# Optimization experiments

Measured on AMD Instinct MI355X. Metric: run time of the kernel, lower is better.

Reference implementation:

```python
import jax, jax.numpy as jnp
import numpy as np

H, DH, ITERS, EPS, LN_EPS = 8, 32, 3, 1e-8, 1e-5

def _ln(x, w, b):
    m = jnp.mean(x, axis=-1, keepdims=True)
    v = jnp.mean(jnp.square(x - m), axis=-1, keepdims=True)
    return (x - m) * jax.lax.rsqrt(v + LN_EPS) * w + b

def setup_inputs() -> dict:
    key = jax.random.key(0)
    ks = jax.random.split(key, 16)
    B, N, D, S = 64, 4096, 256, 8
    DI = H * DH  # 256
    HID = max(D, 128)
    s = 0.02
    return {
        "inputs": jax.random.normal(ks[0], (B, N, D), jnp.float32),
        "noise": jax.random.normal(ks[1], (B, S, D), jnp.float32),
        "slots_mean": jax.random.normal(ks[2], (1, 1, D), jnp.float32),
        "slots_logvar": jax.random.normal(ks[3], (1, 1, D), jnp.float32) * s,
        "wq": jax.random.normal(ks[4], (D, DI), jnp.float32) * s,
        "bq": jnp.zeros((DI,), jnp.float32),
        "wk": jax.random.normal(ks[5], (D, DI), jnp.float32) * s,
        "bk": jnp.zeros((DI,), jnp.float32),
        "wv": jax.random.normal(ks[6], (D, DI), jnp.float32) * s,
        "bv": jnp.zeros((DI,), jnp.float32),
        "wo": jax.random.normal(ks[7], (DI, D), jnp.float32) * s,
        "bo": jnp.zeros((D,), jnp.float32),
        "w_ih": jax.random.normal(ks[8], (D, 3 * D), jnp.float32) * s,
        "b_ih": jnp.zeros((3 * D,), jnp.float32),
        "w_hh": jax.random.normal(ks[9], (D, 3 * D), jnp.float32) * s,
        "b_hh": jnp.zeros((3 * D,), jnp.float32),
        "w1": jax.random.normal(ks[10], (D, HID), jnp.float32) * s,
        "b1": jnp.zeros((HID,), jnp.float32),
        "w2": jax.random.normal(ks[11], (HID, D), jnp.float32) * s,
        "b2": jnp.zeros((D,), jnp.float32),
        "ln_in_w": jnp.ones((D,), jnp.float32), "ln_in_b": jnp.zeros((D,), jnp.float32),
        "ln_s_w": jnp.ones((D,), jnp.float32), "ln_s_b": jnp.zeros((D,), jnp.float32),
        "ln_ff_w": jnp.ones((D,), jnp.float32), "ln_ff_b": jnp.zeros((D,), jnp.float32),
    }

def reference(inputs, noise, slots_mean, slots_logvar, wq, bq, wk, bk, wv, bv,
              wo, bo, w_ih, b_ih, w_hh, b_hh, w1, b1, w2, b2,
              ln_in_w, ln_in_b, ln_s_w, ln_s_b, ln_ff_w, ln_ff_b):
    B, N, D = inputs.shape
    S = noise.shape[1]
    scale = D ** -0.5  # note: scale uses dim, per original code
    # slot init: mean + exp(logvar) * noise (faithful: exp(logvar) used directly)
    slots = slots_mean + jnp.exp(slots_logvar) * noise  # [B,S,D]
    x = _ln(inputs, ln_in_w, ln_in_b)
    k = (x @ wk + bk).reshape(B, N, H, DH).transpose(0, 2, 1, 3)  # [B,H,N,Dh]
    v = (x @ wv + bv).reshape(B, N, H, DH).transpose(0, 2, 1, 3)
    attn = None
    for _ in range(ITERS):
        slots_prev = slots
        s = _ln(slots, ln_s_w, ln_s_b)
        q = (s @ wq + bq).reshape(B, S, H, DH).transpose(0, 2, 1, 3)  # [B,H,S,Dh]
        dots = jnp.einsum('bhid,bhjd->bhij', q, k) * scale  # [B,H,S,N]
        attn = jax.nn.softmax(dots, axis=-2)  # softmax over slot axis
        attn = attn + EPS
        attn = attn / jnp.clip(jnp.sum(attn, axis=-1, keepdims=True), 1e-12)  # L1 over inputs
        upd = jnp.einsum('bhjd,bhij->bhid', v, attn)  # [B,H,S,Dh]
        upd = upd.transpose(0, 2, 1, 3).reshape(B, S, H * DH) @ wo + bo  # [B,S,D]
        # GRUCell (torch gate order r,z,n)
        xg = upd.reshape(B * S, D) @ w_ih + b_ih
        hg = slots_prev.reshape(B * S, D) @ w_hh + b_hh
        xr, xz, xn = jnp.split(xg, 3, axis=-1)
        hr, hz, hn = jnp.split(hg, 3, axis=-1)
        r = jax.nn.sigmoid(xr + hr)
        z = jax.nn.sigmoid(xz + hz)
        n = jnp.tanh(xn + r * hn)
        slots = ((1.0 - z) * n + z * slots_prev.reshape(B * S, D)).reshape(B, S, D)
        ff = _ln(slots, ln_ff_w, ln_ff_b)
        slots = slots + (jax.nn.relu(ff @ w1 + b1) @ w2 + b2)
    return slots, attn
```

## Files before the change

kernel.cpp:

```cpp
#include <hip/hip_runtime.h>
#include <stdint.h>

typedef __attribute__((ext_vector_type(8))) short bf16x8;
typedef __attribute__((ext_vector_type(4))) float f32x4;

__device__ __forceinline__ float b2f(unsigned short s) {
    unsigned int u = ((unsigned int)s) << 16;
    return __builtin_bit_cast(float, u);
}
__device__ __forceinline__ unsigned short f2b(float f) {
    unsigned int u = __builtin_bit_cast(unsigned int, f);
    u += 0x7FFFu + ((u >> 16) & 1u);
    return (unsigned short)(u >> 16);
}
__device__ __forceinline__ void unpack8(uint4 u, float* o) {
    unsigned int a0 = u.x, a1 = u.y, a2 = u.z, a3 = u.w;
    o[0] = __builtin_bit_cast(float, a0 << 16);
    o[1] = __builtin_bit_cast(float, a0 & 0xffff0000u);
    o[2] = __builtin_bit_cast(float, a1 << 16);
    o[3] = __builtin_bit_cast(float, a1 & 0xffff0000u);
    o[4] = __builtin_bit_cast(float, a2 << 16);
    o[5] = __builtin_bit_cast(float, a2 & 0xffff0000u);
    o[6] = __builtin_bit_cast(float, a3 << 16);
    o[7] = __builtin_bit_cast(float, a3 & 0xffff0000u);
}

#define GLOAD_LDS16(g, l) __builtin_amdgcn_global_load_lds( \
    (const __attribute__((address_space(1))) unsigned int*)(g), \
    (__attribute__((address_space(3))) unsigned int*)(l), 16, 0, 0)

#define EPS_ATTN 1e-8f
#define LN_EPS 1e-5f
#define SCALE 0.0625f

__global__ __launch_bounds__(256) void k_prep(const float* __restrict__ wk,
                                              const float* __restrict__ wv,
                                              unsigned short* __restrict__ W3) {
    int g = blockIdx.x * 256 + threadIdx.x;
    int j = g & 7;
    int f = (g >> 3) & 1023;
    int stage = g >> 13;
    int p = f & 15, qq = (f >> 4) & 3, ntl = f >> 6;
    int kc = stage >> 1, half = stage & 1;
    int k = kc * 32 + qq * 8 + j;
    int n = half * 256 + ntl * 16 + p;
    float v = (n < 256) ? wk[k * 256 + n] : wv[k * 256 + (n - 256)];
    W3[g] = f2b(v);
}

__global__ __launch_bounds__(256) void k_init(const float* __restrict__ sm,
                                              const float* __restrict__ slv,
                                              const float* __restrict__ noise,
                                              float* __restrict__ slots) {
    int idx = blockIdx.x * 256 + threadIdx.x;
    int d = idx & 255;
    slots[idx] = sm[d] + expf(slv[d]) * noise[idx];
}

__global__ __launch_bounds__(256, 2) void k_kv(
    const float* __restrict__ x, const float* __restrict__ lnw, const float* __restrict__ lnb,
    const unsigned short* __restrict__ W3, const float* __restrict__ bk, const float* __restrict__ bv,
    unsigned short* __restrict__ Kb, unsigned short* __restrict__ Vb) {
    __shared__ __align__(16) unsigned short sh[33792];
    unsigned short* As = sh;
    unsigned short* Bs = sh + 16384;
    float* bL = (float*)(sh + 32768);
    int t = threadIdx.x;
    int w = t >> 6, lane = t & 63;
    int p = lane & 15, q = lane >> 4;

    {
        const unsigned short* gp = W3 + (size_t)(w * 4) * 512 + lane * 8;
        #pragma unroll
        for (int c = 0; c < 4; ++c)
            GLOAD_LDS16(gp + c * 512, Bs + (w * 4 + c) * 512);
    }
    if (t < 128) {
        float4 bb = (t < 64) ? ((const float4*)bk)[t] : ((const float4*)bv)[t - 64];
        *(float4*)&bL[t * 4] = bb;
    }

    float4 lw  = ((const float4*)lnw)[lane];
    float4 lbv = ((const float4*)lnb)[lane];
    float4 xv[16];
    const float* xbase = x + ((size_t)blockIdx.x * 64 + w * 16) * 256;
    #pragma unroll
    for (int i = 0; i < 16; ++i) xv[i] = ((const float4*)(xbase + i * 256))[lane];
    int kcw = lane >> 3, qw = (lane >> 1) & 3, j0 = (lane & 1) * 4;
    #pragma unroll
    for (int i = 0; i < 16; ++i) {
        float4 v = xv[i];
        float s0 = v.x + v.y + v.z + v.w;
        float s1 = v.x * v.x + v.y * v.y + v.z * v.z + v.w * v.w;
        #pragma unroll
        for (int o = 1; o < 64; o <<= 1) { s0 += __shfl_xor(s0, o); s1 += __shfl_xor(s1, o); }
        float mean = s0 * (1.0f / 256.0f);
        float var  = s1 * (1.0f / 256.0f) - mean * mean;
        float rstd = rsqrtf(var + LN_EPS);
        ushort4 pk;
        pk.x = f2b((v.x - mean) * rstd * lw.x + lbv.x);
        pk.y = f2b((v.y - mean) * rstd * lw.y + lbv.y);
        pk.z = f2b((v.z - mean) * rstd * lw.z + lbv.z);
        pk.w = f2b((v.w - mean) * rstd * lw.w + lbv.w);
        int pos = (qw * 16 + i) ^ kcw;
        *(ushort4*)&As[((w * 8 + kcw) * 64 + pos) * 8 + j0] = pk;
    }
    __syncthreads();

    f32x4 acc[32];
    f32x4 zero = {0.f, 0.f, 0.f, 0.f};
    #pragma unroll
    for (int i = 0; i < 32; ++i) acc[i] = zero;

    for (int s1 = 0; s1 < 16; ++s1) {
        if (s1 < 15) {
            int nx = s1 + 1;
            const unsigned short* gp = W3 + (size_t)nx * 8192 + (w * 4) * 512 + lane * 8;
            unsigned short* lb = Bs + ((nx & 1) ? 8192 : 0);
            #pragma unroll
            for (int c = 0; c < 4; ++c)
                GLOAD_LDS16(gp + c * 512, lb + (w * 4 + c) * 512);
        }
        int kc = s1 >> 1, half = s1 & 1;
        bf16x8 af = *(const bf16x8*)&As[((w * 8 + kc) * 64 + ((q * 16 + p) ^ kc)) * 8];
        const unsigned short* bbuf = Bs + ((s1 & 1) ? 8192 : 0);
        #pragma unroll
        for (int ntl = 0; ntl < 16; ++ntl) {
            bf16x8 bf = *(const bf16x8*)&bbuf[ntl * 512 + lane * 8];
            acc[half * 16 + ntl] = __builtin_amdgcn_mfma_f32_16x16x32_bf16(
                af, bf, acc[half * 16 + ntl], 0, 0, 0);
        }
        __syncthreads();
    }

    unsigned short* rep = As;
    int b_   = blockIdx.x >> 6;
    int n0g  = (blockIdx.x & 63) * 64;

    #pragma unroll
    for (int al = 0; al < 16; ++al) {
        float bias = bL[al * 16 + p];
        int hl = al >> 1, dh = (al & 1) * 16 + p;
        #pragma unroll
        for (int r = 0; r < 4; ++r) {
            int nl = w * 16 + q * 4 + r;
            rep[(hl * 64 + nl) * 32 + dh] = f2b(acc[al][r] + bias);
        }
    }
    __syncthreads();
    #pragma unroll
    for (int i = 0; i < 8; ++i) {
        uint4 vd = *(const uint4*)&rep[(i * 256 + t) * 8];
        *(uint4*)(Kb + (((size_t)b_ * 8 + i) * 4096 + n0g) * 32 + t * 8) = vd;
    }
    #pragma unroll
    for (int al = 0; al < 16; ++al) {
        float bias = bL[256 + al * 16 + p];
        int hl = al >> 1, dh = (al & 1) * 16 + p;
        ushort4 pk;
        pk.x = f2b(acc[16 + al][0] + bias);
        pk.y = f2b(acc[16 + al][1] + bias);
        pk.z = f2b(acc[16 + al][2] + bias);
        pk.w = f2b(acc[16 + al][3] + bias);
        *(ushort4*)(Vb + ((size_t)(b_ * 8 + hl) * 32 + dh) * 4096 + n0g + w * 16 + q * 4) = pk;
    }
}

__global__ __launch_bounds__(256) void k_q(
    const float* __restrict__ slots, const float* __restrict__ lnw, const float* __restrict__ lnb,
    const float* __restrict__ wq, const float* __restrict__ bq, float* __restrict__ qg) {
    __shared__ float sln[256];
    __shared__ float red[8];
    int t = threadIdx.x;
    int row = blockIdx.x;
    float v = slots[(size_t)row * 256 + t];
    float s0 = v, s1 = v * v;
    #pragma unroll
    for (int off = 1; off < 64; off <<= 1) { s0 += __shfl_xor(s0, off); s1 += __shfl_xor(s1, off); }
    if ((t & 63) == 0) { red[t >> 6] = s0; red[4 + (t >> 6)] = s1; }
    __syncthreads();
    float ts0 = red[0] + red[1] + red[2] + red[3];
    float ts1 = red[4] + red[5] + red[6] + red[7];
    float mean = ts0 * (1.f / 256.f);
    float var  = ts1 * (1.f / 256.f) - mean * mean;
    float rstd = rsqrtf(var + LN_EPS);
    sln[t] = (v - mean) * rstd * lnw[t] + lnb[t];
    __syncthreads();
    float acc = bq[t];
    #pragma unroll 4
    for (int k = 0; k < 256; ++k) acc += sln[k] * wq[k * 256 + t];
    int b = row >> 3, sl = row & 7;
    qg[(size_t)b * 2048 + (t >> 5) * 256 + sl * 32 + (t & 31)] = acc;
}

__global__ __launch_bounds__(512) void k_attn(
    const unsigned short* __restrict__ Kg, const unsigned short* __restrict__ VTg,
    const float* __restrict__ qg, float* __restrict__ upd_raw, float* __restrict__ rowsum,
    float* __restrict__ attn_out, int last) {
    __shared__ float supd[8][256];
    __shared__ float srs[8][8];
    int t = threadIdx.x;
    int w = t >> 6, lane = t & 63;
    int c = lane & 15;
    int g = lane >> 4;

    int bh = blockIdx.x;
    const unsigned short* Kbh = Kg  + (size_t)bh * 4096 * 32;
    const unsigned short* Vbh = VTg + (size_t)bh * 32 * 4096;

    bf16x8 qhi = {0,0,0,0,0,0,0,0};
    bf16x8 qlo = {0,0,0,0,0,0,0,0};
    if (c < 8) {
        const float* qp = qg + (size_t)bh * 256 + c * 32 + g * 8;
        #pragma unroll
        for (int j = 0; j < 8; ++j) {
            float qv = qp[j];
            unsigned short hb = f2b(qv);
            qhi[j] = (short)hb;
            qlo[j] = (short)f2b(qv - b2f(hb));
        }
    }

    f32x4 zero = {0.f, 0.f, 0.f, 0.f};
    f32x4 accL = zero, accH = zero;
    float rs = 0.f;
    int nb0 = w * 512;

    #pragma unroll 2
    for (int pr = 0; pr < 16; ++pr) {
        int base = nb0 + pr * 32;
        bf16x8 k0 = *(const bf16x8*)(Kbh + (size_t)(base + c) * 32 + g * 8);
        bf16x8 k1 = *(const bf16x8*)(Kbh + (size_t)(base + 16 + c) * 32 + g * 8);
        const unsigned short* vlo = Vbh + (size_t)c * 4096 + base + g * 4;
        const unsigned short* vhi = Vbh + (size_t)(c + 16) * 4096 + base + g * 4;
        union { ushort4 h[2]; bf16x8 v; } V0, V1;
        V0.h[0] = *(const ushort4*)vlo;
        V0.h[1] = *(const ushort4*)(vlo + 16);
        V1.h[0] = *(const ushort4*)vhi;
        V1.h[1] = *(const ushort4*)(vhi + 16);

        f32x4 s0 = __builtin_amdgcn_mfma_f32_16x16x32_bf16(k0, qhi, zero, 0, 0, 0);
        s0 = __builtin_amdgcn_mfma_f32_16x16x32_bf16(k0, qlo, s0, 0, 0, 0);
        f32x4 s1 = __builtin_amdgcn_mfma_f32_16x16x32_bf16(k1, qhi, zero, 0, 0, 0);
        s1 = __builtin_amdgcn_mfma_f32_16x16x32_bf16(k1, qlo, s1, 0, 0, 0);

        float d0[4], d1[4];
        #pragma unroll
        for (int r = 0; r < 4; ++r) { d0[r] = s0[r] * SCALE; d1[r] = s1[r] * SCALE; }
        float m = fmaxf(fmaxf(fmaxf(d0[0], d0[1]), fmaxf(d0[2], d0[3])),
                        fmaxf(fmaxf(d1[0], d1[1]), fmaxf(d1[2], d1[3])));
        m = fmaxf(m, __shfl_xor(m, 1));
        m = fmaxf(m, __shfl_xor(m, 2));
        m = fmaxf(m, __shfl_xor(m, 4));
        m = fmaxf(m, __shfl_xor(m, 8));
        float a0[4], a1[4];
        #pragma unroll
        for (int r = 0; r < 4; ++r) {
            float e0 = __expf(d0[r] - m);
            float e1 = __expf(d1[r] - m);
            float t0 = e0;
            t0 += __shfl_xor(t0, 1); t0 += __shfl_xor(t0, 2); t0 += __shfl_xor(t0, 4);
            float t1 = e1;
            t1 += __shfl_xor(t1, 1); t1 += __shfl_xor(t1, 2); t1 += __shfl_xor(t1, 4);
            a0[r] = e0 * (1.0f / t0) + EPS_ATTN;
            a1[r] = e1 * (1.0f / t1) + EPS_ATTN;
            rs += a0[r] + a1[r];
        }
        if (last && c < 8) {
            float4 st0 = {a0[0], a0[1], a0[2], a0[3]};
            float4 st1 = {a1[0], a1[1], a1[2], a1[3]};
            float* ap = attn_out + ((size_t)bh * 8 + c) * 4096 + base + g * 4;
            *(float4*)ap = st0;
            *(float4*)(ap + 16) = st1;
        }
        bf16x8 pah, pal;
        float af[8] = {a0[0], a0[1], a0[2], a0[3], a1[0], a1[1], a1[2], a1[3]};
        #pragma unroll
        for (int j = 0; j < 8; ++j) {
            unsigned short hb = f2b(af[j]);
            pah[j] = (short)hb;
            pal[j] = (short)f2b(af[j] - b2f(hb));
        }
        accL = __builtin_amdgcn_mfma_f32_16x16x32_bf16(V0.v, pah, accL, 0, 0, 0);
        accL = __builtin_amdgcn_mfma_f32_16x16x32_bf16(V0.v, pal, accL, 0, 0, 0);
        accH = __builtin_amdgcn_mfma_f32_16x16x32_bf16(V1.v, pah, accH, 0, 0, 0);
        accH = __builtin_amdgcn_mfma_f32_16x16x32_bf16(V1.v, pal, accH, 0, 0, 0);
    }

    rs += __shfl_xor(rs, 16);
    rs += __shfl_xor(rs, 32);
    if (lane < 8) srs[w][lane] = rs;
    if (c < 8) {
        float* up = &supd[w][c * 32 + g * 4];
        up[0]  = accL[0]; up[1]  = accL[1]; up[2]  = accL[2]; up[3]  = accL[3];
        up[16] = accH[0]; up[17] = accH[1]; up[18] = accH[2]; up[19] = accH[3];
    }
    __syncthreads();
    if (t < 256) {
        float v = 0.f;
        #pragma unroll
        for (int ww = 0; ww < 8; ++ww) v += supd[ww][t];
        upd_raw[(size_t)bh * 256 + t] = v;
    }
    if (t < 8) {
        float v = 0.f;
        #pragma unroll
        for (int ww = 0; ww < 8; ++ww) v += srs[ww][t];
        rowsum[bh * 8 + t] = v;
    }
}

__global__ __launch_bounds__(256) void k_gA(
    const float* __restrict__ upd_raw, const float* __restrict__ rowsum,
    const float* __restrict__ wo, const float* __restrict__ bo, float* __restrict__ O) {
    __shared__ float Ul[8][256];
    __shared__ float Pp[4][8][64];
    int t = threadIdx.x;
    int b = blockIdx.x >> 2, cc = blockIdx.x & 3;
    int colbase = cc * 64;
    {
        int r = t >> 5, d0 = (t & 31) * 8;
        int h = d0 >> 5;
        float inv = 1.0f / fmaxf(rowsum[(b * 8 + h) * 8 + r], 1e-12f);
        const float* up = upd_raw + (size_t)(b * 8 + h) * 256 + r * 32 + (d0 & 31);
        float4 u0 = *(const float4*)up;
        float4 u1 = *(const float4*)(up + 4);
        Ul[r][d0 + 0] = u0.x * inv; Ul[r][d0 + 1] = u0.y * inv;
        Ul[r][d0 + 2] = u0.z * inv; Ul[r][d0 + 3] = u0.w * inv;
        Ul[r][d0 + 4] = u1.x * inv; Ul[r][d0 + 5] = u1.y * inv;
        Ul[r][d0 + 6] = u1.z * inv; Ul[r][d0 + 7] = u1.w * inv;
    }
    __syncthreads();
    int c = t & 63, kq = t >> 6;
    float acc[8] = {0.f,0.f,0.f,0.f,0.f,0.f,0.f,0.f};
    const float* wp = wo + (size_t)(kq * 64) * 256 + colbase + c;
    #pragma unroll 16
    for (int k = 0; k < 64; ++k) {
        float wv_ = wp[(size_t)k * 256];
        int kk = kq * 64 + k;
        #pragma unroll
        for (int r = 0; r < 8; ++r) acc[r] += Ul[r][kk] * wv_;
    }
    #pragma unroll
    for (int r = 0; r < 8; ++r) Pp[kq][r][c] = acc[r];
    __syncthreads();
    #pragma unroll
    for (int j = 0; j < 2; ++j) {
        int o = t * 2 + j;
        int r = o >> 6, c2 = o & 63;
        float v = Pp[0][r][c2] + Pp[1][r][c2] + Pp[2][r][c2] + Pp[3][r][c2] + bo[colbase + c2];
        O[(size_t)(b * 8 + r) * 256 + colbase + c2] = v;
    }
}

__global__ __launch_bounds__(256) void k_gB(
    const float* __restrict__ O, const float* __restrict__ slin,
    const float* __restrict__ wih, const float* __restrict__ bih,
    const float* __restrict__ whh, const float* __restrict__ bhh,
    float* __restrict__ gcomb, float* __restrict__ xn, float* __restrict__ hn) {
    __shared__ float Ol[8][256], Hl[8][256];
    __shared__ float Px[2][8][128], Ph[2][8][128];
    int t = threadIdx.x;
    int b = blockIdx.x / 6, cc = blockIdx.x % 6;
    int colbase = cc * 128;
    {
        int r = t >> 5, d0 = (t & 31) * 8;
        const float* op = O + (size_t)(b * 8 + r) * 256 + d0;
        const float* hp = slin + (size_t)(b * 8 + r) * 256 + d0;
        *(float4*)&Ol[r][d0]     = *(const float4*)op;
        *(float4*)&Ol[r][d0 + 4] = *(const float4*)(op + 4);
        *(float4*)&Hl[r][d0]     = *(const float4*)hp;
        *(float4*)&Hl[r][d0 + 4] = *(const float4*)(hp + 4);
    }
    __syncthreads();
    int c = t & 127, kh = t >> 7;
    float ax[8] = {0.f,0.f,0.f,0.f,0.f,0.f,0.f,0.f};
    float ah[8] = {0.f,0.f,0.f,0.f,0.f,0.f,0.f,0.f};
    const float* wxp = wih + (size_t)(kh * 128) * 768 + colbase + c;
    const float* whp = whh + (size_t)(kh * 128) * 768 + colbase + c;
    #pragma unroll 8
    for (int k = 0; k < 128; ++k) {
        float wx = wxp[(size_t)k * 768];
        float wh = whp[(size_t)k * 768];
        int kk = kh * 128 + k;
        #pragma unroll
        for (int r = 0; r < 8; ++r) { ax[r] += Ol[r][kk] * wx; ah[r] += Hl[r][kk] * wh; }
    }
    #pragma unroll
    for (int r = 0; r < 8; ++r) { Px[kh][r][c] = ax[r]; Ph[kh][r][c] = ah[r]; }
    __syncthreads();
    #pragma unroll
    for (int j = 0; j < 4; ++j) {
        int o = t * 4 + j;
        int r = o >> 7, c2 = o & 127;
        int cg = colbase + c2;
        int row = b * 8 + r;
        float vx = Px[0][r][c2] + Px[1][r][c2] + bih[cg];
        float vh = Ph[0][r][c2] + Ph[1][r][c2] + bhh[cg];
        if (cg < 512) {
            gcomb[(size_t)row * 512 + cg] = vx + vh;
        } else {
            xn[(size_t)row * 256 + cg - 512] = vx;
            hn[(size_t)row * 256 + cg - 512] = vh;
        }
    }
}

__global__ __launch_bounds__(256) void k_gC(
    const float* __restrict__ gcomb, const float* __restrict__ xn, const float* __restrict__ hn,
    const float* __restrict__ slin, const float* __restrict__ lnfw, const float* __restrict__ lnfb,
    float* __restrict__ slout, float* __restrict__ F) {
    __shared__ float red[8];
    int t = threadIdx.x, row = blockIdx.x;
    float a_r = gcomb[(size_t)row * 512 + t];
    float a_z = gcomb[(size_t)row * 512 + 256 + t];
    float xnv = xn[(size_t)row * 256 + t];
    float hnv = hn[(size_t)row * 256 + t];
    float hp  = slin[(size_t)row * 256 + t];
    float rg = 1.f / (1.f + expf(-a_r));
    float zg = 1.f / (1.f + expf(-a_z));
    float ng = tanhf(xnv + rg * hnv);
    float s1 = (1.f - zg) * ng + zg * hp;
    slout[(size_t)row * 256 + t] = s1;
    float s0 = s1, sq = s1 * s1;
    #pragma unroll
    for (int o = 1; o < 64; o <<= 1) { s0 += __shfl_xor(s0, o); sq += __shfl_xor(sq, o); }
    if ((t & 63) == 0) { red[t >> 6] = s0; red[4 + (t >> 6)] = sq; }
    __syncthreads();
    float ts0 = red[0] + red[1] + red[2] + red[3];
    float ts1 = red[4] + red[5] + red[6] + red[7];
    float mean = ts0 * (1.f / 256.f);
    float var  = ts1 * (1.f / 256.f) - mean * mean;
    float rstd = rsqrtf(var + LN_EPS);
    F[(size_t)row * 256 + t] = (s1 - mean) * rstd * lnfw[t] + lnfb[t];
}

__global__ __launch_bounds__(256) void k_gD(
    const float* __restrict__ F, const float* __restrict__ w1, const float* __restrict__ b1,
    float* __restrict__ H1) {
    __shared__ float Fl[8][256];
    __shared__ float Pp[4][8][64];
    int t = threadIdx.x;
    int b = blockIdx.x >> 2, cc = blockIdx.x & 3;
    int colbase = cc * 64;
    {
        int r = t >> 5, d0 = (t & 31) * 8;
        const float* fp = F + (size_t)(b * 8 + r) * 256 + d0;
        *(float4*)&Fl[r][d0]     = *(const float4*)fp;
        *(float4*)&Fl[r][d0 + 4] = *(const float4*)(fp + 4);
    }
    __syncthreads();
    int c = t & 63, kq = t >> 6;
    float acc[8] = {0.f,0.f,0.f,0.f,0.f,0.f,0.f,0.f};
    const float* wp = w1 + (size_t)(kq * 64) * 256 + colbase + c;
    #pragma unroll 16
    for (int k = 0; k < 64; ++k) {
        float wv_ = wp[(size_t)k * 256];
        int kk = kq * 64 + k;
        #pragma unroll
        for (int r = 0; r < 8; ++r) acc[r] += Fl[r][kk] * wv_;
    }
    #pragma unroll
    for (int r = 0; r < 8; ++r) Pp[kq][r][c] = acc[r];
    __syncthreads();
    #pragma unroll
    for (int j = 0; j < 2; ++j) {
        int o = t * 2 + j;
        int r = o >> 6, c2 = o & 63;
        float v = Pp[0][r][c2] + Pp[1][r][c2] + Pp[2][r][c2] + Pp[3][r][c2] + b1[colbase + c2];
        H1[(size_t)(b * 8 + r) * 256 + colbase + c2] = fmaxf(v, 0.f);
    }
}

__global__ __launch_bounds__(256) void k_gE(
    const float* __restrict__ H1, const float* __restrict__ w2, const float* __restrict__ b2,
    float* __restrict__ slout) {
    __shared__ float Hl[8][256];
    __shared__ float Pp[4][8][64];
    int t = threadIdx.x;
    int b = blockIdx.x >> 2, cc = blockIdx.x & 3;
    int colbase = cc * 64;
    {
        int r = t >> 5, d0 = (t & 31) * 8;
        const float* hp = H1 + (size_t)(b * 8 + r) * 256 + d0;
        *(float4*)&Hl[r][d0]     = *(const float4*)hp;
        *(float4*)&Hl[r][d0 + 4] = *(const float4*)(hp + 4);
    }
    __syncthreads();
    int c = t & 63, kq = t >> 6;
    float acc[8] = {0.f,0.f,0.f,0.f,0.f,0.f,0.f,0.f};
    const float* wp = w2 + (size_t)(kq * 64) * 256 + colbase + c;
    #pragma unroll 16
    for (int k = 0; k < 64; ++k) {
        float wv_ = wp[(size_t)k * 256];
        int kk = kq * 64 + k;
        #pragma unroll
        for (int r = 0; r < 8; ++r) acc[r] += Hl[r][kk] * wv_;
    }
    #pragma unroll
    for (int r = 0; r < 8; ++r) Pp[kq][r][c] = acc[r];
    __syncthreads();
    #pragma unroll
    for (int j = 0; j < 2; ++j) {
        int o = t * 2 + j;
        int r = o >> 6, c2 = o & 63;
        size_t idx = (size_t)(b * 8 + r) * 256 + colbase + c2;
        float v = Pp[0][r][c2] + Pp[1][r][c2] + Pp[2][r][c2] + Pp[3][r][c2] + b2[colbase + c2];
        slout[idx] = slout[idx] + v;
    }
}

__global__ __launch_bounds__(256) void k_scale(float* __restrict__ attn, const float* __restrict__ rowsum) {
    size_t idx = (size_t)blockIdx.x * 256 + threadIdx.x;
    int row = (int)(idx >> 12);
    float rs = fmaxf(rowsum[row], 1e-12f);
    attn[idx] = attn[idx] / rs;
}

extern "C" void kernel_launch(void* const* d_in, const int* in_sizes, int n_in,
                              void* d_out, int out_size, void* d_ws, size_t ws_size,
                              hipStream_t stream) {
    const float* inputs = (const float*)d_in[0];
    const float* noise  = (const float*)d_in[1];
    const float* sm     = (const float*)d_in[2];
    const float* slv    = (const float*)d_in[3];
    const float* wq     = (const float*)d_in[4];
    const float* bq     = (const float*)d_in[5];
    const float* wk     = (const float*)d_in[6];
    const float* bk     = (const float*)d_in[7];
    const float* wv     = (const float*)d_in[8];
    const float* bv     = (const float*)d_in[9];
    const float* wo     = (const float*)d_in[10];
    const float* bo     = (const float*)d_in[11];
    const float* wih    = (const float*)d_in[12];
    const float* bih    = (const float*)d_in[13];
    const float* whh    = (const float*)d_in[14];
    const float* bhh    = (const float*)d_in[15];
    const float* w1     = (const float*)d_in[16];
    const float* b1     = (const float*)d_in[17];
    const float* w2     = (const float*)d_in[18];
    const float* b2     = (const float*)d_in[19];
    const float* lniw   = (const float*)d_in[20];
    const float* lnib   = (const float*)d_in[21];
    const float* lnsw   = (const float*)d_in[22];
    const float* lnsb   = (const float*)d_in[23];
    const float* lnfw   = (const float*)d_in[24];
    const float* lnfb   = (const float*)d_in[25];

    char* ws = (char*)d_ws;
    unsigned short* Kb = (unsigned short*)ws;
    unsigned short* Vb = (unsigned short*)(ws + 134217728ull);
    float* slotsA  = (float*)(ws + 268435456ull);
    float* slotsB  = (float*)(ws + 268959744ull);
    float* Rr      = (float*)(ws + 269484032ull);
    float* Pr      = (float*)(ws + 270008320ull);
    float* Qr      = (float*)(ws + 270532608ull);
    float* upd_raw = (float*)(ws + 272629760ull);
    float* rowsum  = (float*)(ws + 273154048ull);
    unsigned short* W3 = (unsigned short*)Pr;
    float* O_  = Pr;
    float* gcomb = Qr;
    float* xn = Qr + 262144;
    float* hn = Qr + 393216;
    float* H1 = Qr;
    float* qg = Rr;
    float* F_ = Rr;

    float* out_slots = (float*)d_out;
    float* attn_out  = (float*)d_out + 131072;

    k_prep<<<512, 256, 0, stream>>>(wk, wv, W3);
    k_init<<<512, 256, 0, stream>>>(sm, slv, noise, slotsA);
    k_kv<<<4096, 256, 0, stream>>>(inputs, lniw, lnib, W3, bk, bv, Kb, Vb);
    for (int it = 0; it < 3; ++it) {
        int last = (it == 2);
        float* sl_in  = (it == 0) ? slotsA : ((it == 1) ? slotsB : slotsA);
        float* sl_out = (it == 0) ? slotsB : ((it == 1) ? slotsA : out_slots);
        k_q<<<512, 256, 0, stream>>>(sl_in, lnsw, lnsb, wq, bq, qg);
        k_attn<<<512, 512, 0, stream>>>(Kb, Vb, qg, upd_raw, rowsum, attn_out, last);
        k_gA<<<256, 256, 0, stream>>>(upd_raw, rowsum, wo, bo, O_);
        k_gB<<<384, 256, 0, stream>>>(O_, sl_in, wih, bih, whh, bhh, gcomb, xn, hn);
        k_gC<<<512, 256, 0, stream>>>(gcomb, xn, hn, sl_in, lnfw, lnfb, sl_out, F_);
        k_gD<<<256, 256, 0, stream>>>(F_, w1, b1, H1);
        k_gE<<<256, 256, 0, stream>>>(H1, w2, b2, sl_out);
    }
    k_scale<<<65536, 256, 0, stream>>>(attn_out, rowsum);
}
```

Baseline: 1.057 ms.

## Retile KV projection per-wave over columns, stage V via LDS, vectorize attn scaling

The K/V projection GEMM is reorganized so each wave owns 128 output columns across all 64 rows (4x8 MFMA tiles). B fragments are read directly from global memory instead of being double-buffered into LDS through global_load_lds, which drops the per-step barriers. V output is transposed through a swizzled LDS buffer so it can be written to global as coalesced 16-byte stores instead of scattered 8-byte ones. The final attn normalization kernel now uses float4 loads and a reciprocal multiply instead of a per-element divide. The risk is that direct global B loads have higher latency and are fetched redundantly across waves and blocks.

```diff
diff --git a/kernel.cpp b/kernel.cpp
--- a/kernel.cpp
+++ b/kernel.cpp
@@ -13,21 +13,6 @@
     u += 0x7FFFu + ((u >> 16) & 1u);
     return (unsigned short)(u >> 16);
 }
-__device__ __forceinline__ void unpack8(uint4 u, float* o) {
-    unsigned int a0 = u.x, a1 = u.y, a2 = u.z, a3 = u.w;
-    o[0] = __builtin_bit_cast(float, a0 << 16);
-    o[1] = __builtin_bit_cast(float, a0 & 0xffff0000u);
-    o[2] = __builtin_bit_cast(float, a1 << 16);
-    o[3] = __builtin_bit_cast(float, a1 & 0xffff0000u);
-    o[4] = __builtin_bit_cast(float, a2 << 16);
-    o[5] = __builtin_bit_cast(float, a2 & 0xffff0000u);
-    o[6] = __builtin_bit_cast(float, a3 << 16);
-    o[7] = __builtin_bit_cast(float, a3 & 0xffff0000u);
-}
-
-#define GLOAD_LDS16(g, l) __builtin_amdgcn_global_load_lds( \
-    (const __attribute__((address_space(1))) unsigned int*)(g), \
-    (__attribute__((address_space(3))) unsigned int*)(l), 16, 0, 0)
 
 #define EPS_ATTN 1e-8f
 #define LN_EPS 1e-5f
@@ -41,9 +26,9 @@
     int f = (g >> 3) & 1023;
     int stage = g >> 13;
     int p = f & 15, qq = (f >> 4) & 3, ntl = f >> 6;
-    int kc = stage >> 1, half = stage & 1;
+    int kc = stage >> 1, half_ = stage & 1;
     int k = kc * 32 + qq * 8 + j;
-    int n = half * 256 + ntl * 16 + p;
+    int n = half_ * 256 + ntl * 16 + p;
     float v = (n < 256) ? wk[k * 256 + n] : wv[k * 256 + (n - 256)];
     W3[g] = f2b(v);
 }
@@ -62,19 +47,13 @@
     const unsigned short* __restrict__ W3, const float* __restrict__ bk, const float* __restrict__ bv,
     unsigned short* __restrict__ Kb, unsigned short* __restrict__ Vb) {
     __shared__ __align__(16) unsigned short sh[33792];
-    unsigned short* As = sh;
-    unsigned short* Bs = sh + 16384;
+    unsigned short* As   = sh;
+    unsigned short* repV = sh + 16384;
     float* bL = (float*)(sh + 32768);
     int t = threadIdx.x;
     int w = t >> 6, lane = t & 63;
     int p = lane & 15, q = lane >> 4;
 
-    {
-        const unsigned short* gp = W3 + (size_t)(w * 4) * 512 + lane * 8;
-        #pragma unroll
-        for (int c = 0; c < 4; ++c)
-            GLOAD_LDS16(gp + c * 512, Bs + (w * 4 + c) * 512);
-    }
     if (t < 128) {
         float4 bb = (t < 64) ? ((const float4*)bk)[t] : ((const float4*)bv)[t - 64];
         *(float4*)&bL[t * 4] = bb;
@@ -107,62 +86,79 @@
     }
     __syncthreads();
 
-    f32x4 acc[32];
+    f32x4 acc[4][8];
     f32x4 zero = {0.f, 0.f, 0.f, 0.f};
     #pragma unroll
-    for (int i = 0; i < 32; ++i) acc[i] = zero;
-
-    for (int s1 = 0; s1 < 16; ++s1) {
-        if (s1 < 15) {
-            int nx = s1 + 1;
-            const unsigned short* gp = W3 + (size_t)nx * 8192 + (w * 4) * 512 + lane * 8;
-            unsigned short* lb = Bs + ((nx & 1) ? 8192 : 0);
+    for (int rt = 0; rt < 4; ++rt)
+        #pragma unroll
+        for (int ct = 0; ct < 8; ++ct) acc[rt][ct] = zero;
+
+    const unsigned short* Wb = W3 + (size_t)(w >> 1) * 8192 + (size_t)((w & 1) * 8) * 512 + lane * 8;
+    #pragma unroll 2
+    for (int kc = 0; kc < 8; ++kc) {
+        bf16x8 af[4];
+        #pragma unroll
+        for (int rt = 0; rt < 4; ++rt)
+            af[rt] = *(const bf16x8*)&As[((rt * 8 + kc) * 64 + ((q * 16 + p) ^ kc)) * 8];
+        #pragma unroll
+        for (int ct = 0; ct < 8; ++ct) {
+            bf16x8 bf = *(const bf16x8*)(Wb + (size_t)kc * 16384 + ct * 512);
             #pragma unroll
-            for (int c = 0; c < 4; ++c)
-                GLOAD_LDS16(gp + c * 512, lb + (w * 4 + c) * 512);
-        }
-        int kc = s1 >> 1, half = s1 & 1;
-        bf16x8 af = *(const bf16x8*)&As[((w * 8 + kc) * 64 + ((q * 16 + p) ^ kc)) * 8];
-        const unsigned short* bbuf = Bs + ((s1 & 1) ? 8192 : 0);
-        #pragma unroll
-        for (int ntl = 0; ntl < 16; ++ntl) {
-            bf16x8 bf = *(const bf16x8*)&bbuf[ntl * 512 + lane * 8];
-            acc[half * 16 + ntl] = __builtin_amdgcn_mfma_f32_16x16x32_bf16(
-                af, bf, acc[half * 16 + ntl], 0, 0, 0);
-        }
-        __syncthreads();
-    }
-
-    unsigned short* rep = As;
-    int b_   = blockIdx.x >> 6;
-    int n0g  = (blockIdx.x & 63) * 64;
-
-    #pragma unroll
-    for (int al = 0; al < 16; ++al) {
-        float bias = bL[al * 16 + p];
-        int hl = al >> 1, dh = (al & 1) * 16 + p;
-        #pragma unroll
-        for (int r = 0; r < 4; ++r) {
-            int nl = w * 16 + q * 4 + r;
-            rep[(hl * 64 + nl) * 32 + dh] = f2b(acc[al][r] + bias);
-        }
-    }
-    __syncthreads();
+            for (int rt = 0; rt < 4; ++rt)
+                acc[rt][ct] = __builtin_amdgcn_mfma_f32_16x16x32_bf16(af[rt], bf, acc[rt][ct], 0, 0, 0);
+        }
+    }
+    __syncthreads();
+
+    unsigned short* repK = As;
+    int b_  = blockIdx.x >> 6;
+    int n0g = (blockIdx.x & 63) * 64;
+
+    if (w < 2) {
+        #pragma unroll
+        for (int ct = 0; ct < 8; ++ct) {
+            int col = w * 128 + ct * 16 + p;
+            float bias = bL[col];
+            int hl = col >> 5, dh = col & 31;
+            #pragma unroll
+            for (int rt = 0; rt < 4; ++rt) {
+                #pragma unroll
+                for (int r = 0; r < 4; ++r) {
+                    int nl = rt * 16 + q * 4 + r;
+                    repK[(hl * 64 + nl) * 32 + dh] = f2b(acc[rt][ct][r] + bias);
+                }
+            }
+        }
+    } else {
+        #pragma unroll
+        for (int ct = 0; ct < 8; ++ct) {
+            int vrow = (w - 2) * 128 + ct * 16 + p;
+            float bias = bL[256 + vrow];
+            #pragma unroll
+            for (int rt = 0; rt < 4; ++rt) {
+                int chunk = (rt * 4 + q) ^ (p & 14);
+                ushort4 pk;
+                pk.x = f2b(acc[rt][ct][0] + bias);
+                pk.y = f2b(acc[rt][ct][1] + bias);
+                pk.z = f2b(acc[rt][ct][2] + bias);
+                pk.w = f2b(acc[rt][ct][3] + bias);
+                *(ushort4*)&repV[vrow * 64 + chunk * 4] = pk;
+            }
+        }
+    }
+    __syncthreads();
+
     #pragma unroll
     for (int i = 0; i < 8; ++i) {
-        uint4 vd = *(const uint4*)&rep[(i * 256 + t) * 8];
+        uint4 vd = *(const uint4*)&repK[(i * 256 + t) * 8];
         *(uint4*)(Kb + (((size_t)b_ * 8 + i) * 4096 + n0g) * 32 + t * 8) = vd;
     }
     #pragma unroll
-    for (int al = 0; al < 16; ++al) {
-        float bias = bL[256 + al * 16 + p];
-        int hl = al >> 1, dh = (al & 1) * 16 + p;
-        ushort4 pk;
-        pk.x = f2b(acc[16 + al][0] + bias);
-        pk.y = f2b(acc[16 + al][1] + bias);
-        pk.z = f2b(acc[16 + al][2] + bias);
-        pk.w = f2b(acc[16 + al][3] + bias);
-        *(ushort4*)(Vb + ((size_t)(b_ * 8 + hl) * 32 + dh) * 4096 + n0g + w * 16 + q * 4) = pk;
+    for (int i = 0; i < 8; ++i) {
+        int vrow = i * 32 + (t >> 3);
+        int c16 = t & 7;
+        uint4 vd = *(const uint4*)&repV[vrow * 64 + ((2 * c16) ^ (vrow & 14)) * 4];
+        *(uint4*)(Vb + ((size_t)(b_ * 8 + (vrow >> 5)) * 32 + (vrow & 31)) * 4096 + n0g + c16 * 8) = vd;
     }
 }
 
@@ -511,10 +507,12 @@
 }
 
 __global__ __launch_bounds__(256) void k_scale(float* __restrict__ attn, const float* __restrict__ rowsum) {
-    size_t idx = (size_t)blockIdx.x * 256 + threadIdx.x;
-    int row = (int)(idx >> 12);
-    float rs = fmaxf(rowsum[row], 1e-12f);
-    attn[idx] = attn[idx] / rs;
+    size_t i4 = ((size_t)blockIdx.x * 256 + threadIdx.x) * 4;
+    int row = (int)(i4 >> 12);
+    float inv = 1.0f / fmaxf(rowsum[row], 1e-12f);
+    float4 v = *(float4*)(attn + i4);
+    v.x *= inv; v.y *= inv; v.z *= inv; v.w *= inv;
+    *(float4*)(attn + i4) = v;
 }
 
 extern "C" void kernel_launch(void* const* d_in, const int* in_sizes, int n_in,
@@ -584,5 +582,5 @@
         k_gD<<<256, 256, 0, stream>>>(F_, w1, b1, H1);
         k_gE<<<256, 256, 0, stream>>>(H1, w2, b2, sl_out);
     }
-    k_scale<<<65536, 256, 0, stream>>>(attn_out, rowsum);
-}
+    k_scale<<<16384, 256, 0, stream>>>(attn_out, rowsum);
+}
```

Result: no change. 1.068 ms (+1.0%).
